# Kernel optimization log

Hardware: AMD Instinct MI355X
Metric: run time of the kernel (lower is better)

The kernel has to match this reference:

```python
import jax, jax.numpy as jnp
import numpy as np

B = 4096
N0 = 784          # MNIST input
L0 = 263          # fc0: Gather chain 784 -> 256 (ELU after each)
L2 = 121          # fc2: Gather chain 256 -> 12 (ELU after each); final Gather 12 -> 10 has no ELU


def _win3(x):
    # x: (B, N) -> (B, N-2, 3) sliding windows of width 3
    return jnp.stack([x[:, :-2], x[:, 1:-1], x[:, 2:]], axis=-1)


def setup_inputs() -> dict:
    key = jax.random.key(0)
    kx, k0, k1, k2, k3, k4 = jax.random.split(key, 6)
    s = 0.75  # keeps activation variance roughly stable through ~380 ELU glia layers
    x = jax.random.normal(kx, (B, N0), jnp.float32)
    W0 = jax.random.normal(k0, (L0, 782, 3), jnp.float32) * s
    m0 = np.arange(782)[None, :] < (780 - 2 * np.arange(L0))[:, None]
    W0 = W0 * jnp.asarray(m0[..., None], jnp.float32)  # zero out rows past each layer's out size
    Ws = jax.random.normal(k1, (256, 3), jnp.float32) * s
    bs = jax.random.normal(k2, (256,), jnp.float32) * 0.1
    W2 = jax.random.normal(k3, (L2, 254, 3), jnp.float32) * s
    m2 = np.arange(254)[None, :] < (252 - 2 * np.arange(L2))[:, None]
    W2 = W2 * jnp.asarray(m2[..., None], jnp.float32)
    Wlast = jax.random.normal(k4, (10, 3), jnp.float32) * s
    return {"x": x, "W0": W0, "Ws": Ws, "bs": bs, "W2": W2, "Wlast": Wlast}


def reference(x, W0, Ws, bs, W2, Wlast):
    def gather_step(h, W):
        # locally-connected width-3 Gather (out = in - 2, bias=False) + ELU.
        # Invalid tail rows of W are zero, so padded positions stay exactly 0
        # (ELU(0)=0) and never contaminate valid windows.
        y = jax.nn.elu(jnp.einsum('bjk,jk->bj', _win3(h), W))
        return jnp.pad(y, ((0, 0), (0, 2))), None

    # fc0: 263 Gather+ELU layers, 784 -> 256 (valid prefix of fixed-width state)
    h, _ = jax.lax.scan(gather_step, x, W0)
    h = h[:, :256]
    # fc1: Slide(256) + ELU -- same-size width-3 locally connected layer, zero-padded window, bias
    hp = jnp.pad(h, ((0, 0), (1, 1)))
    h = jax.nn.elu(jnp.einsum('bjk,jk->bj', _win3(hp), Ws) + bs)
    # fc2: 121 Gather+ELU layers, 256 -> 12
    h, _ = jax.lax.scan(gather_step, h, W2)
    # final Gather(12): 12 -> 10, no ELU
    logits = jnp.einsum('bjk,jk->bj', _win3(h[:, :12]), Wlast)
    return jax.nn.log_softmax(logits, axis=1)
```

## Files before the change

kernel.cpp:

```cpp
#include <hip/hip_runtime.h>
#include <math.h>


#define G 2

template<int HI>
__device__ __forceinline__ float2 pk_mul_b(float2 a, float2 w) {
    float2 d;
    if constexpr (HI)
        asm("v_pk_mul_f32 %0, %1, %2 op_sel:[0,1] op_sel_hi:[1,1]"
            : "=v"(d) : "v"(a), "v"(w));
    else
        asm("v_pk_mul_f32 %0, %1, %2 op_sel_hi:[1,0]"
            : "=v"(d) : "v"(a), "v"(w));
    return d;
}
template<int HI>
__device__ __forceinline__ float2 pk_fma_b(float2 a, float2 w, float2 c) {
    float2 d;
    if constexpr (HI)
        asm("v_pk_fma_f32 %0, %1, %2, %3 op_sel:[0,1,0] op_sel_hi:[1,1,1]"
            : "=v"(d) : "v"(a), "v"(w), "v"(c));
    else
        asm("v_pk_fma_f32 %0, %1, %2, %3 op_sel_hi:[1,0,1]"
            : "=v"(d) : "v"(a), "v"(w), "v"(c));
    return d;
}
__device__ __forceinline__ float2 pk_mul2(float2 a, float2 b) {
    float2 d;
    asm("v_pk_mul_f32 %0, %1, %2" : "=v"(d) : "v"(a), "v"(b));
    return d;
}
__device__ __forceinline__ float vexp2(float x) {
    float d;
    asm("v_exp_f32 %0, %1" : "=v"(d) : "v"(x));
    return d;
}

__device__ __forceinline__ float elu_f(float a) {
    return a > 0.0f ? a : (__expf(a) - 1.0f);
}

template<int K, int I, int NW>
__device__ __forceinline__ void slot_run(float2 (&h)[K], const float2 (&w)[NW],
                                         float2 e0, float2 e1, float2 l2e) {
    if constexpr (I < K) {
        float2 x1, x2;
        if constexpr (I + 1 < K) x1 = h[I + 1]; else x1 = e0;
        if constexpr (I + 2 < K) x2 = h[I + 2];
        else if constexpr (I + 2 == K) x2 = e0;
        else x2 = e1;
        float2 acc = pk_mul_b<(3 * I + 2) & 1>(x2, w[(3 * I + 2) >> 1]);
        acc = pk_fma_b<(3 * I + 1) & 1>(x1, w[(3 * I + 1) >> 1], acc);
        acc = pk_fma_b<(3 * I) & 1>(h[I], w[(3 * I) >> 1], acc);
        float2 t = pk_mul2(acc, l2e);
        float ex = vexp2(t.x) - 1.0f;
        float ey = vexp2(t.y) - 1.0f;
        h[I].x = acc.x > 0.0f ? acc.x : ex;
        h[I].y = acc.y > 0.0f ? acc.y : ey;
        slot_run<K, I + 1, NW>(h, w, e0, e1, l2e);
    }
}

template<int K, int NW>
__device__ __forceinline__ void scan_layer_pk(float2 (&h)[K], const float2 (&w)[NW],
                                              float2 l2e) {
    float2 e0, e1;
    e0.x = __shfl_down(h[0].x, 1); e0.y = __shfl_down(h[0].y, 1);
    if constexpr (K >= 2) { e1.x = __shfl_down(h[1].x, 1); e1.y = __shfl_down(h[1].y, 1); }
    else                  { e1.x = __shfl_down(h[0].x, 2); e1.y = __shfl_down(h[0].y, 2); }
    slot_run<K, 0, NW>(h, w, e0, e1, l2e);
}

template<int NC>
__device__ __forceinline__ void load_wt2(float2 (&w)[2 * NC], const float4* __restrict__ Tp,
                                         int lr) {
#pragma unroll
    for (int c = 0; c < NC; ++c) {
        float4 v = Tp[(size_t)lr * (NC * 64) + c * 64];
        w[2 * c]     = make_float2(v.x, v.y);
        w[2 * c + 1] = make_float2(v.z, v.w);
    }
}

template<int K, int NC, int NL>
__device__ __forceinline__ void scan_phase_pk(const float* __restrict__ Tphase,
                                              int lane, float2 (&h)[K], float2 l2e) {
    static_assert(NL >= 3, "ring needs >=3 layers");
    const float4* __restrict__ Tp = reinterpret_cast<const float4*>(Tphase) + lane;
    float2 w0[2 * NC], w1[2 * NC], w2[2 * NC];
    load_wt2<NC>(w0, Tp, 0);
    load_wt2<NC>(w1, Tp, 1);
    load_wt2<NC>(w2, Tp, 2);
    int l = 0;
    for (; l + 3 <= NL; l += 3) {
        scan_layer_pk<K>(h, w0, l2e);  load_wt2<NC>(w0, Tp, l + 3);
        scan_layer_pk<K>(h, w1, l2e);  load_wt2<NC>(w1, Tp, l + 4);
        scan_layer_pk<K>(h, w2, l2e);  load_wt2<NC>(w2, Tp, l + 5);
    }
    if constexpr (NL % 3 >= 1) scan_layer_pk<K>(h, w0, l2e);
    if constexpr (NL % 3 >= 2) scan_layer_pk<K>(h, w1, l2e);
}

template<int KA, int KB>
__device__ __forceinline__ void repack_pk(float2 (&a)[KA], float2 (&n)[KB],
                                          float2* lds, int lane) {
    __syncthreads();
#pragma unroll
    for (int i = 0; i < KA; ++i) lds[KA * lane + i] = a[i];
    __syncthreads();
#pragma unroll
    for (int i = 0; i < KB; ++i) n[i] = lds[KB * lane + i];
    __syncthreads();
}

__device__ __forceinline__ void stage2_pk(float2 (&h)[5], const float* __restrict__ Ws,
                                          const float* __restrict__ bs, int lane) {
#pragma unroll
    for (int i = 0; i < 5; ++i)
        if (5 * lane + i > 255) h[i] = make_float2(0.f, 0.f);
    float w0[5], w1[5], w2[5], bb[5];
#pragma unroll
    for (int i = 0; i < 5; ++i) {
        int j = 5 * lane + i;
        bool v = j < 256;
        w0[i] = v ? Ws[3 * j + 0] : 0.f;
        w1[i] = v ? Ws[3 * j + 1] : 0.f;
        w2[i] = v ? Ws[3 * j + 2] : 0.f;
        bb[i] = v ? bs[j] : 0.f;
    }
    float2 p, q;
    p.x = __shfl_up(h[4].x, 1); p.y = __shfl_up(h[4].y, 1);
    if (lane == 0) p = make_float2(0.f, 0.f);
    q.x = __shfl_down(h[0].x, 1); q.y = __shfl_down(h[0].y, 1);
    float2 y[5];
#pragma unroll
    for (int i = 0; i < 5; ++i) {
        float2 xm = (i == 0) ? p : h[i - 1];
        float2 xp = (i == 4) ? q : h[i + 1];
        float ax = fmaf(xm.x, w0[i], fmaf(h[i].x, w1[i], fmaf(xp.x, w2[i], bb[i])));
        float ay = fmaf(xm.y, w0[i], fmaf(h[i].y, w1[i], fmaf(xp.y, w2[i], bb[i])));
        y[i].x = elu_f(ax);
        y[i].y = elu_f(ay);
    }
#pragma unroll
    for (int i = 0; i < 5; ++i) h[i] = y[i];
}

__device__ __forceinline__ void emit_row(float v, const float* __restrict__ Wl,
                                         float* __restrict__ out, int row, int lane) {
    float n1 = __shfl_down(v, 1);
    float n2 = __shfl_down(v, 2);
    float lg = 0.0f;
    if (lane < 10)
        lg = fmaf(v, Wl[3 * lane], fmaf(n1, Wl[3 * lane + 1], n2 * Wl[3 * lane + 2]));
    float t = (lane < 10) ? lg : -1e30f;
#pragma unroll
    for (int d = 1; d < 16; d <<= 1) t = fmaxf(t, __shfl_xor(t, d));
    float e = (lane < 10) ? __expf(lg - t) : 0.0f;
    float s = e;
#pragma unroll
    for (int d = 1; d < 16; d <<= 1) s += __shfl_xor(s, d);
    float lse = t + __logf(s);
    if (lane < 10) out[(size_t)row * 10 + lane] = lg - lse;
}

#define T_TOTAL 531712
#define T_ALLOC (T_TOTAL + 512)

__global__ __launch_bounds__(256)
void reorder_w(const float* __restrict__ W0, const float* __restrict__ W2,
               float* __restrict__ T) {
    int idx = blockIdx.x * 256 + threadIdx.x;
    if (idx >= T_ALLOC) return;
    if (idx >= T_TOTAL) { T[idx] = 0.0f; return; }
    int base, l0, K, NC, s1;
    if      (idx < 17920)  { base = 0;      l0 = 0;   K = 13; NC = 10; s1 = 1; }
    else if (idx < 91648)  { base = 17920;  l0 = 7;   K = 12; NC = 9;  s1 = 1; }
    else if (idx < 165376) { base = 91648;  l0 = 39;  K = 11; NC = 9;  s1 = 1; }
    else if (idx < 230912) { base = 165376; l0 = 71;  K = 10; NC = 8;  s1 = 1; }
    else if (idx < 288256) { base = 230912; l0 = 103; K = 9;  NC = 7;  s1 = 1; }
    else if (idx < 337408) { base = 288256; l0 = 135; K = 8;  NC = 6;  s1 = 1; }
    else if (idx < 386560) { base = 337408; l0 = 167; K = 7;  NC = 6;  s1 = 1; }
    else if (idx < 427520) { base = 386560; l0 = 199; K = 6;  NC = 5;  s1 = 1; }
    else if (idx < 460288) { base = 427520; l0 = 231; K = 5;  NC = 4;  s1 = 1; }
    else if (idx < 484096) { base = 460288; l0 = 0;   K = 4;  NC = 3;  s1 = 0; }
    else if (idx < 508672) { base = 484096; l0 = 31;  K = 3;  NC = 3;  s1 = 0; }
    else if (idx < 525056) { base = 508672; l0 = 63;  K = 2;  NC = 2;  s1 = 0; }
    else                   { base = 525056; l0 = 95;  K = 1;  NC = 1;  s1 = 0; }
    const float* Wsrc = s1 ? W0 : W2;
    int lstride = s1 ? 2346 : 762;
    int rel  = idx - base;
    int perL = NC * 256;
    int lr   = rel / perL;
    int r2   = rel - lr * perL;
    int c    = r2 >> 8;
    int ln   = (r2 >> 2) & 63;
    int f    = r2 & 3;
    int elem = 4 * c + f;
    float v = 0.0f;
    if (elem < 3 * K) {
        int b = 3 * K * ln;
        if (b + 3 * K > lstride) b = lstride - 3 * K;
        v = Wsrc[(size_t)(l0 + lr) * lstride + b + elem];
    }
    T[idx] = v;
}

__global__ __launch_bounds__(64)
void pg_kernel_pk(const float* __restrict__ x,  const float* __restrict__ Ws,
                  const float* __restrict__ bs, const float* __restrict__ Wlast,
                  const float* __restrict__ T,  float* __restrict__ out)
{
    __shared__ float2 lds2[13 * 64];
    const int lane = threadIdx.x;
    const int rowA = blockIdx.x * G;
    const int rowB = rowA + 1;
    const float2 l2e = make_float2(1.44269504088896340736f, 1.44269504088896340736f);

    float2 h13[13];
#pragma unroll
    for (int i = 0; i < 13; ++i) {
        int p = 13 * lane + i;
        h13[i].x = (p < 784) ? x[(size_t)rowA * 784 + p] : 0.0f;
        h13[i].y = (p < 784) ? x[(size_t)rowB * 784 + p] : 0.0f;
    }

    scan_phase_pk<13, 10, 7>(T + 0,       lane, h13, l2e);
    float2 h12[12]; repack_pk<13, 12>(h13, h12, lds2, lane);
    scan_phase_pk<12, 9, 32>(T + 17920,   lane, h12, l2e);
    float2 h11[11]; repack_pk<12, 11>(h12, h11, lds2, lane);
    scan_phase_pk<11, 9, 32>(T + 91648,   lane, h11, l2e);
    float2 h10[10]; repack_pk<11, 10>(h11, h10, lds2, lane);
    scan_phase_pk<10, 8, 32>(T + 165376,  lane, h10, l2e);
    float2 h9[9];   repack_pk<10, 9>(h10, h9, lds2, lane);
    scan_phase_pk<9, 7, 32>(T + 230912,   lane, h9, l2e);
    float2 h8[8];   repack_pk<9, 8>(h9, h8, lds2, lane);
    scan_phase_pk<8, 6, 32>(T + 288256,   lane, h8, l2e);
    float2 h7[7];   repack_pk<8, 7>(h8, h7, lds2, lane);
    scan_phase_pk<7, 6, 32>(T + 337408,   lane, h7, l2e);
    float2 h6[6];   repack_pk<7, 6>(h7, h6, lds2, lane);
    scan_phase_pk<6, 5, 32>(T + 386560,   lane, h6, l2e);
    float2 h5[5];   repack_pk<6, 5>(h6, h5, lds2, lane);
    scan_phase_pk<5, 4, 32>(T + 427520,   lane, h5, l2e);

    stage2_pk(h5, Ws, bs, lane);

    float2 h4[4];   repack_pk<5, 4>(h5, h4, lds2, lane);
    scan_phase_pk<4, 3, 31>(T + 460288,   lane, h4, l2e);
    float2 h3[3];   repack_pk<4, 3>(h4, h3, lds2, lane);
    scan_phase_pk<3, 3, 32>(T + 484096,   lane, h3, l2e);
    float2 h2[2];   repack_pk<3, 2>(h3, h2, lds2, lane);
    scan_phase_pk<2, 2, 32>(T + 508672,   lane, h2, l2e);
    float2 h1[1];   repack_pk<2, 1>(h2, h1, lds2, lane);
    scan_phase_pk<1, 1, 26>(T + 525056,   lane, h1, l2e);

    emit_row(h1[0].x, Wlast, out, rowA, lane);
    emit_row(h1[0].y, Wlast, out, rowB, lane);
}

template<int K>
__device__ __forceinline__ void scan_layer_s(float (&h)[K], const float (&w)[3 * K]) {
    float e0 = __shfl_down(h[0], 1);
    float e1;
    if constexpr (K >= 2) e1 = __shfl_down(h[1], 1);
    else                  e1 = __shfl_down(h[0], 2);
#pragma unroll
    for (int i = 0; i < K; ++i) {
        float x1 = (i + 1 < K) ? h[i + 1] : e0;
        float x2 = (i + 2 < K) ? h[i + 2] : ((i + 2 == K) ? e0 : e1);
        float a = fmaf(h[i], w[3 * i], fmaf(x1, w[3 * i + 1], x2 * w[3 * i + 2]));
        h[i] = elu_f(a);
    }
}
template<int K>
__device__ __forceinline__ void scan_phase_s(const float* __restrict__ W, int lstride,
                                             int l0, int l1, int lane,
                                             float (&hA)[K], float (&hB)[K]) {
    int base = 3 * K * lane;
    if (base + 3 * K > lstride) base = lstride - 3 * K;
    const float* __restrict__ Wp = W + (size_t)l0 * lstride + base;
    float wa[3 * K];
    for (int l = l0; l < l1; ++l) {
#pragma unroll
        for (int j = 0; j < 3 * K; ++j) wa[j] = Wp[j];
        scan_layer_s<K>(hA, wa);
        scan_layer_s<K>(hB, wa);
        Wp += lstride;
    }
}
template<int KA, int KB>
__device__ __forceinline__ void repack_s(float (&aA)[KA], float (&aB)[KA],
                                         float (&nA)[KB], float (&nB)[KB],
                                         float* lds, int lane) {
    __syncthreads();
#pragma unroll
    for (int i = 0; i < KA; ++i) lds[KA * lane + i] = aA[i];
    __syncthreads();
#pragma unroll
    for (int i = 0; i < KB; ++i) nA[i] = lds[KB * lane + i];
    __syncthreads();
#pragma unroll
    for (int i = 0; i < KA; ++i) lds[KA * lane + i] = aB[i];
    __syncthreads();
#pragma unroll
    for (int i = 0; i < KB; ++i) nB[i] = lds[KB * lane + i];
    __syncthreads();
}
__global__ __launch_bounds__(64)
void pg_kernel_d(const float* __restrict__ x,  const float* __restrict__ W0,
                 const float* __restrict__ Ws, const float* __restrict__ bs,
                 const float* __restrict__ W2, const float* __restrict__ Wlast,
                 float* __restrict__ out)
{
    __shared__ float lds[13 * 64];
    const int lane = threadIdx.x;
    const int rowA = blockIdx.x * 2;
    const int rowB = rowA + 1;
    float a13[13], b13[13];
#pragma unroll
    for (int i = 0; i < 13; ++i) {
        int p = 13 * lane + i;
        a13[i] = (p < 784) ? x[(size_t)rowA * 784 + p] : 0.0f;
        b13[i] = (p < 784) ? x[(size_t)rowB * 784 + p] : 0.0f;
    }
    scan_phase_s<13>(W0, 2346, 0, 71, lane, a13, b13);
    float a10[10], b10[10]; repack_s<13, 10>(a13, b13, a10, b10, lds, lane);
    scan_phase_s<10>(W0, 2346, 71, 167, lane, a10, b10);
    float a7[7], b7[7];     repack_s<10, 7>(a10, b10, a7, b7, lds, lane);
    scan_phase_s<7>(W0, 2346, 167, 231, lane, a7, b7);
    float a5[5], b5[5];     repack_s<7, 5>(a7, b7, a5, b5, lds, lane);
    scan_phase_s<5>(W0, 2346, 231, 263, lane, a5, b5);
    {
        float2 hp[5];
#pragma unroll
        for (int i = 0; i < 5; ++i) hp[i] = make_float2(a5[i], b5[i]);
        stage2_pk(hp, Ws, bs, lane);
#pragma unroll
        for (int i = 0; i < 5; ++i) { a5[i] = hp[i].x; b5[i] = hp[i].y; }
    }
    float a4[4], b4[4];     repack_s<5, 4>(a5, b5, a4, b4, lds, lane);
    scan_phase_s<4>(W2, 762, 0, 31, lane, a4, b4);
    float a3[3], b3[3];     repack_s<4, 3>(a4, b4, a3, b3, lds, lane);
    scan_phase_s<3>(W2, 762, 31, 63, lane, a3, b3);
    float a2_[2], b2_[2];   repack_s<3, 2>(a3, b3, a2_, b2_, lds, lane);
    scan_phase_s<2>(W2, 762, 63, 95, lane, a2_, b2_);
    float a1[1], b1[1];     repack_s<2, 1>(a2_, b2_, a1, b1, lds, lane);
    scan_phase_s<1>(W2, 762, 95, 121, lane, a1, b1);
    emit_row(a1[0], Wlast, out, rowA, lane);
    emit_row(b1[0], Wlast, out, rowB, lane);
}

extern "C" void kernel_launch(void* const* d_in, const int* in_sizes, int n_in,
                              void* d_out, int out_size, void* d_ws, size_t ws_size,
                              hipStream_t stream) {
    const float* x     = (const float*)d_in[0];
    const float* W0    = (const float*)d_in[1];
    const float* Ws    = (const float*)d_in[2];
    const float* bs    = (const float*)d_in[3];
    const float* W2    = (const float*)d_in[4];
    const float* Wlast = (const float*)d_in[5];
    float* out = (float*)d_out;

    if (ws_size >= (size_t)T_ALLOC * sizeof(float)) {
        float* T = (float*)d_ws;
        reorder_w<<<(T_ALLOC + 255) / 256, 256, 0, stream>>>(W0, W2, T);
        pg_kernel_pk<<<4096 / G, 64, 0, stream>>>(x, Ws, bs, Wlast, T, out);
    } else {
        pg_kernel_d<<<2048, 64, 0, stream>>>(x, W0, Ws, bs, W2, Wlast, out);
    }
}
```

Baseline: 237.3 us.

## Split each row pair's layer chain across two wavefronts with overlapping halos

Each block now runs two 64-lane wavefronts that each own half of the activation vector, with an overlapping halo. This halves the per-lane slot count (7 instead of 13 at the start), which cuts the serial per-layer work and register pressure. The halos are re-exchanged through LDS every 32 layers, and the weight reorder is widened to hold per-wavefront weight slices. The cost is some redundant computation in the overlap region, extra block-level barriers, and a larger reordered-weight workspace.

```diff
diff --git a/kernel.cpp b/kernel.cpp
--- a/kernel.cpp
+++ b/kernel.cpp
@@ -72,79 +72,55 @@
     slot_run<K, 0, NW>(h, w, e0, e1, l2e);
 }
 
-template<int NC>
+template<int NC, int LS>
 __device__ __forceinline__ void load_wt2(float2 (&w)[2 * NC], const float4* __restrict__ Tp,
                                          int lr) {
 #pragma unroll
     for (int c = 0; c < NC; ++c) {
-        float4 v = Tp[(size_t)lr * (NC * 64) + c * 64];
+        float4 v = Tp[(size_t)lr * LS + c * 64];
         w[2 * c]     = make_float2(v.x, v.y);
         w[2 * c + 1] = make_float2(v.z, v.w);
     }
 }
 
 template<int K, int NC, int NL>
-__device__ __forceinline__ void scan_phase_pk(const float* __restrict__ Tphase,
-                                              int lane, float2 (&h)[K], float2 l2e) {
+__device__ __forceinline__ void scan_phase_split(const float* __restrict__ Tphase,
+                                                 int w, int lane, float2 (&h)[K],
+                                                 float2 l2e) {
     static_assert(NL >= 3, "ring needs >=3 layers");
-    const float4* __restrict__ Tp = reinterpret_cast<const float4*>(Tphase) + lane;
+    constexpr int LS = 2 * NC * 64;
+    const float4* __restrict__ Tp =
+        reinterpret_cast<const float4*>(Tphase) + (size_t)w * (NC * 64) + lane;
     float2 w0[2 * NC], w1[2 * NC], w2[2 * NC];
-    load_wt2<NC>(w0, Tp, 0);
-    load_wt2<NC>(w1, Tp, 1);
-    load_wt2<NC>(w2, Tp, 2);
+    load_wt2<NC, LS>(w0, Tp, 0);
+    load_wt2<NC, LS>(w1, Tp, 1);
+    load_wt2<NC, LS>(w2, Tp, 2);
     int l = 0;
     for (; l + 3 <= NL; l += 3) {
-        scan_layer_pk<K>(h, w0, l2e);  load_wt2<NC>(w0, Tp, l + 3);
-        scan_layer_pk<K>(h, w1, l2e);  load_wt2<NC>(w1, Tp, l + 4);
-        scan_layer_pk<K>(h, w2, l2e);  load_wt2<NC>(w2, Tp, l + 5);
+        scan_layer_pk<K>(h, w0, l2e);  load_wt2<NC, LS>(w0, Tp, l + 3);
+        scan_layer_pk<K>(h, w1, l2e);  load_wt2<NC, LS>(w1, Tp, l + 4);
+        scan_layer_pk<K>(h, w2, l2e);  load_wt2<NC, LS>(w2, Tp, l + 5);
     }
     if constexpr (NL % 3 >= 1) scan_layer_pk<K>(h, w0, l2e);
     if constexpr (NL % 3 >= 2) scan_layer_pk<K>(h, w1, l2e);
 }
 
 template<int KA, int KB>
-__device__ __forceinline__ void repack_pk(float2 (&a)[KA], float2 (&n)[KB],
-                                          float2* lds, int lane) {
-    __syncthreads();
-#pragma unroll
-    for (int i = 0; i < KA; ++i) lds[KA * lane + i] = a[i];
-    __syncthreads();
-#pragma unroll
-    for (int i = 0; i < KB; ++i) n[i] = lds[KB * lane + i];
-    __syncthreads();
-}
-
-__device__ __forceinline__ void stage2_pk(float2 (&h)[5], const float* __restrict__ Ws,
-                                          const float* __restrict__ bs, int lane) {
-#pragma unroll
-    for (int i = 0; i < 5; ++i)
-        if (5 * lane + i > 255) h[i] = make_float2(0.f, 0.f);
-    float w0[5], w1[5], w2[5], bb[5];
-#pragma unroll
-    for (int i = 0; i < 5; ++i) {
-        int j = 5 * lane + i;
-        bool v = j < 256;
-        w0[i] = v ? Ws[3 * j + 0] : 0.f;
-        w1[i] = v ? Ws[3 * j + 1] : 0.f;
-        w2[i] = v ? Ws[3 * j + 2] : 0.f;
-        bb[i] = v ? bs[j] : 0.f;
-    }
-    float2 p, q;
-    p.x = __shfl_up(h[4].x, 1); p.y = __shfl_up(h[4].y, 1);
-    if (lane == 0) p = make_float2(0.f, 0.f);
-    q.x = __shfl_down(h[0].x, 1); q.y = __shfl_down(h[0].y, 1);
-    float2 y[5];
-#pragma unroll
-    for (int i = 0; i < 5; ++i) {
-        float2 xm = (i == 0) ? p : h[i - 1];
-        float2 xp = (i == 4) ? q : h[i + 1];
-        float ax = fmaf(xm.x, w0[i], fmaf(h[i].x, w1[i], fmaf(xp.x, w2[i], bb[i])));
-        float ay = fmaf(xm.y, w0[i], fmaf(h[i].y, w1[i], fmaf(xp.y, w2[i], bb[i])));
-        y[i].x = elu_f(ax);
-        y[i].y = elu_f(ay);
-    }
-#pragma unroll
-    for (int i = 0; i < 5; ++i) h[i] = y[i];
+__device__ __forceinline__ void repack_split(float2 (&a)[KA], float2 (&n)[KB],
+                                             float2* lds, int w, int lane) {
+    constexpr int HA = 64 * KA - 64;
+    constexpr int HB = 64 * KB - 64;
+    __syncthreads();
+    int p0 = w * HA + KA * lane;
+#pragma unroll
+    for (int i = 0; i < KA; ++i) {
+        int p = p0 + i;
+        if (w == 1 || p < HA) lds[p] = a[i];
+    }
+    __syncthreads();
+    int q0 = w * HB + KB * lane;
+#pragma unroll
+    for (int i = 0; i < KB; ++i) n[i] = lds[q0 + i];
 }
 
 __device__ __forceinline__ void emit_row(float v, const float* __restrict__ Wl,
@@ -165,8 +141,8 @@
     if (lane < 10) out[(size_t)row * 10 + lane] = lg - lse;
 }
 
-#define T_TOTAL 531712
-#define T_ALLOC (T_TOTAL + 512)
+#define T_TOTAL 728064
+#define T_ALLOC (T_TOTAL + 1024)
 
 __global__ __launch_bounds__(256)
 void reorder_w(const float* __restrict__ W0, const float* __restrict__ W2,
@@ -175,88 +151,126 @@
     if (idx >= T_ALLOC) return;
     if (idx >= T_TOTAL) { T[idx] = 0.0f; return; }
     int base, l0, K, NC, s1;
-    if      (idx < 17920)  { base = 0;      l0 = 0;   K = 13; NC = 10; s1 = 1; }
-    else if (idx < 91648)  { base = 17920;  l0 = 7;   K = 12; NC = 9;  s1 = 1; }
-    else if (idx < 165376) { base = 91648;  l0 = 39;  K = 11; NC = 9;  s1 = 1; }
-    else if (idx < 230912) { base = 165376; l0 = 71;  K = 10; NC = 8;  s1 = 1; }
-    else if (idx < 288256) { base = 230912; l0 = 103; K = 9;  NC = 7;  s1 = 1; }
-    else if (idx < 337408) { base = 288256; l0 = 135; K = 8;  NC = 6;  s1 = 1; }
-    else if (idx < 386560) { base = 337408; l0 = 167; K = 7;  NC = 6;  s1 = 1; }
-    else if (idx < 427520) { base = 386560; l0 = 199; K = 6;  NC = 5;  s1 = 1; }
-    else if (idx < 460288) { base = 427520; l0 = 231; K = 5;  NC = 4;  s1 = 1; }
-    else if (idx < 484096) { base = 460288; l0 = 0;   K = 4;  NC = 3;  s1 = 0; }
-    else if (idx < 508672) { base = 484096; l0 = 31;  K = 3;  NC = 3;  s1 = 0; }
-    else if (idx < 525056) { base = 508672; l0 = 63;  K = 2;  NC = 2;  s1 = 0; }
-    else                   { base = 525056; l0 = 95;  K = 1;  NC = 1;  s1 = 0; }
+    if      (idx < 98304)  { base = 0;      l0 = 0;   K = 7; NC = 6; s1 = 1; }
+    else if (idx < 196608) { base = 98304;  l0 = 32;  K = 7; NC = 6; s1 = 1; }
+    else if (idx < 278528) { base = 196608; l0 = 64;  K = 6; NC = 5; s1 = 1; }
+    else if (idx < 360448) { base = 278528; l0 = 96;  K = 6; NC = 5; s1 = 1; }
+    else if (idx < 425984) { base = 360448; l0 = 128; K = 5; NC = 4; s1 = 1; }
+    else if (idx < 491520) { base = 425984; l0 = 160; K = 5; NC = 4; s1 = 1; }
+    else if (idx < 540672) { base = 491520; l0 = 192; K = 4; NC = 3; s1 = 1; }
+    else if (idx < 589824) { base = 540672; l0 = 224; K = 4; NC = 3; s1 = 1; }
+    else if (idx < 600576) { base = 589824; l0 = 256; K = 3; NC = 3; s1 = 1; }
+    else if (idx < 649728) { base = 600576; l0 = 0;   K = 3; NC = 3; s1 = 0; }
+    else if (idx < 682496) { base = 649728; l0 = 32;  K = 2; NC = 2; s1 = 0; }
+    else if (idx < 715264) { base = 682496; l0 = 64;  K = 2; NC = 2; s1 = 0; }
+    else                   { base = 715264; l0 = 96;  K = 1; NC = 1; s1 = 0; }
     const float* Wsrc = s1 ? W0 : W2;
     int lstride = s1 ? 2346 : 762;
     int rel  = idx - base;
-    int perL = NC * 256;
+    int perL = 2 * NC * 256;
     int lr   = rel / perL;
     int r2   = rel - lr * perL;
-    int c    = r2 >> 8;
-    int ln   = (r2 >> 2) & 63;
-    int f    = r2 & 3;
+    int w    = r2 / (NC * 256);
+    int r3   = r2 - w * (NC * 256);
+    int c    = r3 >> 8;
+    int ln   = (r3 >> 2) & 63;
+    int f    = r3 & 3;
     int elem = 4 * c + f;
     float v = 0.0f;
     if (elem < 3 * K) {
-        int b = 3 * K * ln;
+        int H = 64 * K - 64;
+        int b = 3 * (w * H + K * ln);
         if (b + 3 * K > lstride) b = lstride - 3 * K;
         v = Wsrc[(size_t)(l0 + lr) * lstride + b + elem];
     }
     T[idx] = v;
 }
 
-__global__ __launch_bounds__(64)
-void pg_kernel_pk(const float* __restrict__ x,  const float* __restrict__ Ws,
-                  const float* __restrict__ bs, const float* __restrict__ Wlast,
-                  const float* __restrict__ T,  float* __restrict__ out)
+__global__ __launch_bounds__(128, 4)
+void pg_split(const float* __restrict__ x,  const float* __restrict__ Ws,
+              const float* __restrict__ bs, const float* __restrict__ Wlast,
+              const float* __restrict__ T,  float* __restrict__ out)
 {
-    __shared__ float2 lds2[13 * 64];
-    const int lane = threadIdx.x;
+    __shared__ float2 lds[832];
+    const int t    = threadIdx.x;
+    const int w    = t >> 6;
+    const int lane = t & 63;
     const int rowA = blockIdx.x * G;
     const int rowB = rowA + 1;
     const float2 l2e = make_float2(1.44269504088896340736f, 1.44269504088896340736f);
-
-    float2 h13[13];
-#pragma unroll
-    for (int i = 0; i < 13; ++i) {
-        int p = 13 * lane + i;
-        h13[i].x = (p < 784) ? x[(size_t)rowA * 784 + p] : 0.0f;
-        h13[i].y = (p < 784) ? x[(size_t)rowB * 784 + p] : 0.0f;
-    }
-
-    scan_phase_pk<13, 10, 7>(T + 0,       lane, h13, l2e);
-    float2 h12[12]; repack_pk<13, 12>(h13, h12, lds2, lane);
-    scan_phase_pk<12, 9, 32>(T + 17920,   lane, h12, l2e);
-    float2 h11[11]; repack_pk<12, 11>(h12, h11, lds2, lane);
-    scan_phase_pk<11, 9, 32>(T + 91648,   lane, h11, l2e);
-    float2 h10[10]; repack_pk<11, 10>(h11, h10, lds2, lane);
-    scan_phase_pk<10, 8, 32>(T + 165376,  lane, h10, l2e);
-    float2 h9[9];   repack_pk<10, 9>(h10, h9, lds2, lane);
-    scan_phase_pk<9, 7, 32>(T + 230912,   lane, h9, l2e);
-    float2 h8[8];   repack_pk<9, 8>(h9, h8, lds2, lane);
-    scan_phase_pk<8, 6, 32>(T + 288256,   lane, h8, l2e);
-    float2 h7[7];   repack_pk<8, 7>(h8, h7, lds2, lane);
-    scan_phase_pk<7, 6, 32>(T + 337408,   lane, h7, l2e);
-    float2 h6[6];   repack_pk<7, 6>(h7, h6, lds2, lane);
-    scan_phase_pk<6, 5, 32>(T + 386560,   lane, h6, l2e);
-    float2 h5[5];   repack_pk<6, 5>(h6, h5, lds2, lane);
-    scan_phase_pk<5, 4, 32>(T + 427520,   lane, h5, l2e);
-
-    stage2_pk(h5, Ws, bs, lane);
-
-    float2 h4[4];   repack_pk<5, 4>(h5, h4, lds2, lane);
-    scan_phase_pk<4, 3, 31>(T + 460288,   lane, h4, l2e);
-    float2 h3[3];   repack_pk<4, 3>(h4, h3, lds2, lane);
-    scan_phase_pk<3, 3, 32>(T + 484096,   lane, h3, l2e);
-    float2 h2[2];   repack_pk<3, 2>(h3, h2, lds2, lane);
-    scan_phase_pk<2, 2, 32>(T + 508672,   lane, h2, l2e);
-    float2 h1[1];   repack_pk<2, 1>(h2, h1, lds2, lane);
-    scan_phase_pk<1, 1, 26>(T + 525056,   lane, h1, l2e);
-
-    emit_row(h1[0].x, Wlast, out, rowA, lane);
-    emit_row(h1[0].y, Wlast, out, rowB, lane);
+    const float2 z2  = make_float2(0.0f, 0.0f);
+
+    float2 h7[7];
+    {
+        int p0 = w * 384 + 7 * lane;
+#pragma unroll
+        for (int i = 0; i < 7; ++i) {
+            int p = p0 + i;
+            h7[i].x = (p < 784) ? x[(size_t)rowA * 784 + p] : 0.0f;
+            h7[i].y = (p < 784) ? x[(size_t)rowB * 784 + p] : 0.0f;
+        }
+    }
+
+    scan_phase_split<7, 6, 32>(T + 0,      w, lane, h7, l2e);
+    repack_split<7, 7>(h7, h7, lds, w, lane);
+    scan_phase_split<7, 6, 32>(T + 98304, w, lane, h7, l2e);
+    float2 h6[6]; repack_split<7, 6>(h7, h6, lds, w, lane);
+    scan_phase_split<6, 5, 32>(T + 196608, w, lane, h6, l2e);
+    repack_split<6, 6>(h6, h6, lds, w, lane);
+    scan_phase_split<6, 5, 32>(T + 278528, w, lane, h6, l2e);
+    float2 h5[5]; repack_split<6, 5>(h6, h5, lds, w, lane);
+    scan_phase_split<5, 4, 32>(T + 360448, w, lane, h5, l2e);
+    repack_split<5, 5>(h5, h5, lds, w, lane);
+    scan_phase_split<5, 4, 32>(T + 425984, w, lane, h5, l2e);
+    float2 h4[4]; repack_split<5, 4>(h5, h4, lds, w, lane);
+    scan_phase_split<4, 3, 32>(T + 491520, w, lane, h4, l2e);
+    repack_split<4, 4>(h4, h4, lds, w, lane);
+    scan_phase_split<4, 3, 32>(T + 540672, w, lane, h4, l2e);
+    float2 h3[3]; repack_split<4, 3>(h4, h3, lds, w, lane);
+    scan_phase_split<3, 3, 7>(T + 589824, w, lane, h3, l2e);
+
+    __syncthreads();
+    {
+        int p0 = w * 128 + 3 * lane;
+#pragma unroll
+        for (int i = 0; i < 3; ++i) {
+            int p = p0 + i;
+            if (w == 1 || p < 128) lds[p] = h3[i];
+        }
+    }
+    __syncthreads();
+    {
+        int p0 = w * 128 + 3 * lane;
+        float2 y[3];
+#pragma unroll
+        for (int i = 0; i < 3; ++i) {
+            int j = p0 + i;
+            if (j < 256) {
+                float2 hm = (j > 0)   ? lds[j - 1] : z2;
+                float2 hc = lds[j];
+                float2 hp = (j < 255) ? lds[j + 1] : z2;
+                float w0 = Ws[3 * j], w1 = Ws[3 * j + 1], w2 = Ws[3 * j + 2];
+                float b = bs[j];
+                y[i].x = elu_f(fmaf(hm.x, w0, fmaf(hc.x, w1, fmaf(hp.x, w2, b))));
+                y[i].y = elu_f(fmaf(hm.y, w0, fmaf(hc.y, w1, fmaf(hp.y, w2, b))));
+            } else y[i] = z2;
+        }
+#pragma unroll
+        for (int i = 0; i < 3; ++i) h3[i] = y[i];
+    }
+
+    scan_phase_split<3, 3, 32>(T + 600576, w, lane, h3, l2e);
+    float2 h2[2]; repack_split<3, 2>(h3, h2, lds, w, lane);
+    scan_phase_split<2, 2, 32>(T + 649728, w, lane, h2, l2e);
+    repack_split<2, 2>(h2, h2, lds, w, lane);
+    scan_phase_split<2, 2, 32>(T + 682496, w, lane, h2, l2e);
+    float2 h1[1]; repack_split<2, 1>(h2, h1, lds, w, lane);
+    scan_phase_split<1, 1, 25>(T + 715264, w, lane, h1, l2e);
+
+    if (w == 0) {
+        emit_row(h1[0].x, Wlast, out, rowA, lane);
+        emit_row(h1[0].y, Wlast, out, rowB, lane);
+    }
 }
 
 template<int K>
@@ -332,12 +346,28 @@
     float a5[5], b5[5];     repack_s<7, 5>(a7, b7, a5, b5, lds, lane);
     scan_phase_s<5>(W0, 2346, 231, 263, lane, a5, b5);
     {
-        float2 hp[5];
-#pragma unroll
-        for (int i = 0; i < 5; ++i) hp[i] = make_float2(a5[i], b5[i]);
-        stage2_pk(hp, Ws, bs, lane);
-#pragma unroll
-        for (int i = 0; i < 5; ++i) { a5[i] = hp[i].x; b5[i] = hp[i].y; }
+        float ya[5], yb[5];
+        float pa = __shfl_up(a5[4], 1); if (lane == 0) pa = 0.f;
+        float pb = __shfl_up(b5[4], 1); if (lane == 0) pb = 0.f;
+        float qa = __shfl_down(a5[0], 1);
+        float qb = __shfl_down(b5[0], 1);
+#pragma unroll
+        for (int i = 0; i < 5; ++i) {
+            int j = 5 * lane + i;
+            bool v = j < 256;
+            float w0 = v ? Ws[3 * j] : 0.f, w1 = v ? Ws[3 * j + 1] : 0.f;
+            float w2 = v ? Ws[3 * j + 2] : 0.f, b = v ? bs[j] : 0.f;
+            float am = (i == 0) ? pa : a5[i - 1];
+            float ap = (i == 4) ? qa : a5[i + 1];
+            float bm = (i == 0) ? pb : b5[i - 1];
+            float bp = (i == 4) ? qb : b5[i + 1];
+            float ac = v ? a5[i] : 0.f, bc = v ? b5[i] : 0.f;
+            if (!v) { am = ap = bm = bp = 0.f; }
+            ya[i] = elu_f(fmaf(am, w0, fmaf(ac, w1, fmaf(ap, w2, b))));
+            yb[i] = elu_f(fmaf(bm, w0, fmaf(bc, w1, fmaf(bp, w2, b))));
+        }
+#pragma unroll
+        for (int i = 0; i < 5; ++i) { a5[i] = ya[i]; b5[i] = yb[i]; }
     }
     float a4[4], b4[4];     repack_s<5, 4>(a5, b5, a4, b4, lds, lane);
     scan_phase_s<4>(W2, 762, 0, 31, lane, a4, b4);
@@ -365,7 +395,7 @@
     if (ws_size >= (size_t)T_ALLOC * sizeof(float)) {
         float* T = (float*)d_ws;
         reorder_w<<<(T_ALLOC + 255) / 256, 256, 0, stream>>>(W0, W2, T);
-        pg_kernel_pk<<<4096 / G, 64, 0, stream>>>(x, Ws, bs, Wlast, T, out);
+        pg_split<<<4096 / G, 128, 0, stream>>>(x, Ws, bs, Wlast, T, out);
     } else {
         pg_kernel_d<<<2048, 64, 0, stream>>>(x, W0, Ws, bs, W2, Wlast, out);
     }
```

Result: slower. 249.8 us (+5.3%).
